# Kernel tuning notes

Hardware: AMD Instinct MI355X
Metric: run time of the kernel (lower is better)

## Reference

```python
import jax, jax.numpy as jnp
import numpy as np
from jax import lax

B, CIN, COUT, H, W = 4, 192, 192, 256, 256
K, S, P = 3, 1, 1


def setup_inputs() -> dict:
    key = jax.random.key(0)
    k1, k2, k3, k4 = jax.random.split(key, 4)
    x = jax.random.normal(k1, (B, CIN, H, W), dtype=jnp.float32)
    mask = jax.random.randint(k2, (B, 1, H, W), 0, 2, dtype=jnp.int32)
    fan_in = CIN * K * K
    bound = 1.0 / np.sqrt(fan_in)
    weight = jax.random.uniform(k3, (COUT, CIN, K, K), dtype=jnp.float32, minval=-bound, maxval=bound)
    bias = jax.random.uniform(k4, (COUT,), dtype=jnp.float32, minval=-bound, maxval=bound)
    return {"x": x, "mask": mask, "weight": weight, "bias": bias}


def reference(x, mask, weight, bias):
    # Dense conv (NCHW, OIHW). Equivalent to the unfold + matmul on gathered
    # patches; the custom scatter kernel writes results only at output
    # positions whose receptive field overlaps a nonzero mask entry,
    # leaving other positions zero.
    out = lax.conv_general_dilated(
        x, weight,
        window_strides=(S, S),
        padding=[(P, P), (P, P)],
        dimension_numbers=("NCHW", "OIHW", "NCHW"),
    ) + bias[None, :, None, None]

    # valid[b, 0, oh, ow] = any(mask patch != 0)  -> max-pool of (mask != 0)
    m = jnp.any(mask != 0, axis=1, keepdims=True).astype(out.dtype)  # [B,1,H,W]
    pooled = lax.reduce_window(
        m, 0.0, lax.max,
        window_dimensions=(1, 1, K, K),
        window_strides=(1, 1, S, S),
        padding=[(0, 0), (0, 0), (P, P), (P, P)],
    )  # [B,1,Hout,Wout]
    valid = (pooled > 0).astype(out.dtype)
    return out * valid
```

## Files before the change

### kernel.cpp

```cpp
#include <hip/hip_runtime.h>

typedef short short8 __attribute__((ext_vector_type(8)));
typedef __bf16 bf16x8 __attribute__((ext_vector_type(8)));
typedef float f32x4 __attribute__((ext_vector_type(4)));

#define HP 258

__device__ __forceinline__ short f2bf(float f) {
  unsigned u = __builtin_bit_cast(unsigned, f);
  unsigned r = u + 0x7fffu + ((u >> 16) & 1u);
  return (short)(r >> 16);
}

__device__ __forceinline__ void async16(void* l, const void* g) {
  __builtin_amdgcn_global_load_lds((const __attribute__((address_space(1))) void*)g,
                                   (__attribute__((address_space(3))) void*)l,
                                   16, 0, 0);
}

__global__ __launch_bounds__(256) void zero_border(short* __restrict__ Xp) {
  int gid = blockIdx.x * 256 + threadIdx.x;
  if (gid >= 4 * 1028 * 24) return;
  int g = gid % 24;
  int pix = gid / 24;
  int b = pix / 1028;
  int i = pix - b * 1028;
  int h, w;
  if (i < 258)      { h = 0;   w = i; }
  else if (i < 516) { h = 257; w = i - 258; }
  else { int j = i - 516; h = 1 + (j >> 1); w = (j & 1) ? 257 : 0; }
  short8 z = {0, 0, 0, 0, 0, 0, 0, 0};
  *(short8*)&Xp[(((size_t)b * HP + h) * HP + w) * 192 + g * 8] = z;
}

__global__ __launch_bounds__(256) void transpose_x(const float* __restrict__ x,
                                                   short* __restrict__ Xp) {
  __shared__ short lds[64 * 200];
  const int t = threadIdx.x;
  const int w = t & 63;
  const int g = t >> 6;
  const int w0 = blockIdx.x << 6;
  const int ih = blockIdx.y;
  const int b = blockIdx.z;
  const float* xb = x + ((size_t)b * 192) * 65536 + (size_t)ih * 256 + w0;
#pragma unroll
  for (int pass = 0; pass < 6; ++pass) {
    int ci = pass * 32 + g * 8;
    short8 v;
#pragma unroll
    for (int j = 0; j < 8; ++j) v[j] = f2bf(xb[(size_t)(ci + j) * 65536 + w]);
    *(short8*)&lds[w * 200 + ci] = v;
  }
  __syncthreads();
  short* dst = Xp + (((size_t)b * HP + (ih + 1)) * HP + (w0 + 1)) * 192;
#pragma unroll
  for (int i = 0; i < 6; ++i) {
    int gid = i * 256 + t;
    int ww = gid / 24;
    int c = gid - ww * 24;
    short8 vv = *(const short8*)&lds[ww * 200 + c * 8];
    *(short8*)&dst[(size_t)ww * 192 + c * 8] = vv;
  }
}

__global__ __launch_bounds__(256) void repack_w(const float* __restrict__ Wsrc,
                                                short* __restrict__ Wr) {
  int gid = blockIdx.x * 256 + threadIdx.x;
  if (gid >= 9 * 6 * 768) return;
  int gr = gid % 768;
  int tk = gid / 768;
  int kc = tk % 6;
  int tap = tk / 6;
  int co = gr >> 2;
  int q = (gr & 3) ^ (co & 3);
  int ci = kc * 32 + q * 8;
  short8 v;
#pragma unroll
  for (int j = 0; j < 8; ++j) v[j] = f2bf(Wsrc[(size_t)(co * 192 + ci + j) * 9 + tap]);
  *(short8*)&Wr[(size_t)gid * 8] = v;
}

__global__ __launch_bounds__(256) void valid_mask(const int* __restrict__ mask,
                                                  float* __restrict__ Vg) {
  int gid = blockIdx.x * 256 + threadIdx.x;
  int b = gid >> 16;
  int r = gid & 65535;
  int oh = r >> 8;
  int ow = r & 255;
  const int* mb = mask + ((size_t)b << 16);
  int any = 0;
  for (int dh = -1; dh <= 1; ++dh) {
    int h = oh + dh;
    if ((unsigned)h >= 256u) continue;
    for (int dw = -1; dw <= 1; ++dw) {
      int w = ow + dw;
      if ((unsigned)w >= 256u) continue;
      any |= (mb[h * 256 + w] != 0);
    }
  }
  Vg[gid] = any ? 1.0f : 0.0f;
}

__global__ __launch_bounds__(256) void conv_mfma(
    const short* __restrict__ Xp,
    const short* __restrict__ Wr,
    const float* __restrict__ Vg,
    const float* __restrict__ bias,
    float* __restrict__ out)
{
  __shared__ short Al[768 * 8];
  __shared__ short Bl[512 * 8];

  const int t = threadIdx.x;
  const int lane = t & 63;
  const int wave = t >> 6;
  const int quad = lane >> 4;
  const int l16 = lane & 15;

  const int b = blockIdx.z;
  const int oh = blockIdx.y;
  const int ow0 = blockIdx.x << 7;

  const int axor = quad ^ (l16 & 3);
  int aoff[3];
#pragma unroll
  for (int c = 0; c < 3; ++c) aoff[c] = ((wave * 48 + c * 16 + l16) * 4 + axor) * 8;
  int boff[8];
#pragma unroll
  for (int s = 0; s < 8; ++s) boff[s] = ((s * 16 + l16) * 4 + axor) * 8;

  const int p0 = t >> 2;
  const int q0 = (t & 3) ^ (p0 & 3);

  const f32x4 fzero = {0.f, 0.f, 0.f, 0.f};
  f32x4 acc[3][8];
#pragma unroll
  for (int c = 0; c < 3; ++c)
#pragma unroll
    for (int s = 0; s < 8; ++s) acc[c][s] = fzero;

  const short* Xb = Xp + (size_t)b * HP * HP * 192;

  for (int kh = 0; kh < 3; ++kh) {
    for (int kw = 0; kw < 3; ++kw) {
      const int tap = kh * 3 + kw;
      const short* Wt = Wr + (size_t)tap * 6 * 768 * 8;
      const short* Xrow = Xb + ((size_t)(oh + kh) * HP + (ow0 + kw)) * 192;
      const short* xs0 = Xrow + p0 * 192 + q0 * 8;
      for (int kc = 0; kc < 6; ++kc) {
        const short* wsrc = Wt + kc * (768 * 8) + t * 8;
        async16(&Al[t * 8], wsrc);
        async16(&Al[(t + 256) * 8], wsrc + 256 * 8);
        async16(&Al[(t + 512) * 8], wsrc + 512 * 8);
        const short* xsrc = xs0 + kc * 32;
        async16(&Bl[t * 8], xsrc);
        async16(&Bl[(t + 256) * 8], xsrc + 64 * 192);
        __syncthreads();

        short8 a[3], bb[8];
#pragma unroll
        for (int c = 0; c < 3; ++c) a[c] = *(const short8*)&Al[aoff[c]];
#pragma unroll
        for (int s = 0; s < 8; ++s) bb[s] = *(const short8*)&Bl[boff[s]];
#pragma unroll
        for (int c = 0; c < 3; ++c)
#pragma unroll
          for (int s = 0; s < 8; ++s)
            acc[c][s] = __builtin_amdgcn_mfma_f32_16x16x32_bf16(
                __builtin_bit_cast(bf16x8, a[c]), __builtin_bit_cast(bf16x8, bb[s]),
                acc[c][s], 0, 0, 0);
        __syncthreads();
      }
    }
  }

  float bv[3][4];
#pragma unroll
  for (int c = 0; c < 3; ++c)
#pragma unroll
    for (int r = 0; r < 4; ++r) bv[c][r] = bias[wave * 48 + c * 16 + quad * 4 + r];

  const float* vrow = Vg + ((size_t)b * 256 + oh) * 256 + ow0;
  float* ob = out + (size_t)(b * 192) * 65536 + (size_t)oh * 256 + ow0;
#pragma unroll
  for (int s = 0; s < 8; ++s) {
    float v = vrow[s * 16 + l16];
#pragma unroll
    for (int c = 0; c < 3; ++c) {
      int cobase = wave * 48 + c * 16 + quad * 4;
#pragma unroll
      for (int r = 0; r < 4; ++r)
        ob[(size_t)(cobase + r) * 65536 + s * 16 + l16] = (acc[c][s][r] + bv[c][r]) * v;
    }
  }
}

__global__ __launch_bounds__(256) void naive_conv(
    const float* __restrict__ x, const int* __restrict__ mask,
    const float* __restrict__ w, const float* __restrict__ bias,
    float* __restrict__ out) {
  size_t gid = (size_t)blockIdx.x * 256 + threadIdx.x;
  int ow = (int)(gid & 255);
  int oh = (int)((gid >> 8) & 255);
  int rest = (int)(gid >> 16);
  int co = rest % 192;
  int b = rest / 192;
  int any = 0;
  for (int dh = -1; dh <= 1; ++dh) {
    int h = oh + dh;
    if ((unsigned)h >= 256u) continue;
    for (int dw = -1; dw <= 1; ++dw) {
      int ww2 = ow + dw;
      if ((unsigned)ww2 >= 256u) continue;
      any |= (mask[((size_t)b << 16) + h * 256 + ww2] != 0);
    }
  }
  if (!any) { out[gid] = 0.f; return; }
  float acc = bias[co];
  const float* xb = x + (size_t)b * 192 * 65536;
  const float* wc = w + (size_t)co * 192 * 9;
  for (int ci = 0; ci < 192; ++ci) {
    const float* xc = xb + (size_t)ci * 65536;
    const float* wk = wc + ci * 9;
    for (int kh = 0; kh < 3; ++kh) {
      int h = oh + kh - 1;
      if ((unsigned)h >= 256u) continue;
      for (int kw = 0; kw < 3; ++kw) {
        int w2 = ow + kw - 1;
        if ((unsigned)w2 >= 256u) continue;
        acc += xc[h * 256 + w2] * wk[kh * 3 + kw];
      }
    }
  }
  out[gid] = acc;
}

extern "C" void kernel_launch(void* const* d_in, const int* in_sizes, int n_in,
                              void* d_out, int out_size, void* d_ws, size_t ws_size,
                              hipStream_t stream) {
  const float* x = (const float*)d_in[0];
  const int* mask = (const int*)d_in[1];
  const float* w = (const float*)d_in[2];
  const float* bias = (const float*)d_in[3];
  float* out = (float*)d_out;

  const size_t xp_bytes = (size_t)4 * HP * HP * 192 * 2;
  const size_t wr_bytes = (size_t)9 * 6 * 768 * 8 * 2;
  const size_t vg_bytes = (size_t)4 * 256 * 256 * 4;

  if (d_ws && ws_size >= xp_bytes + wr_bytes + vg_bytes) {
    short* Xp = (short*)d_ws;
    short* Wr = (short*)((char*)d_ws + xp_bytes);
    float* Vg = (float*)((char*)d_ws + xp_bytes + wr_bytes);
    zero_border<<<386, 256, 0, stream>>>(Xp);
    transpose_x<<<dim3(4, 256, 4), 256, 0, stream>>>(x, Xp);
    repack_w<<<162, 256, 0, stream>>>(w, Wr);
    valid_mask<<<1024, 256, 0, stream>>>(mask, Vg);
    conv_mfma<<<dim3(2, 256, 4), 256, 0, stream>>>(Xp, Wr, Vg, bias, out);
  } else {
    naive_conv<<<196608, 256, 0, stream>>>(x, mask, w, bias, out);
  }
}
```

Before: 556.0 us.

## Fuse prep kernels into one launch and double-buffer conv LDS staging

New measurement: 593.7 us. +6.8%, slower.

```diff
diff --git a/kernel.cpp b/kernel.cpp
--- a/kernel.cpp
+++ b/kernel.cpp
@@ -18,87 +18,97 @@
                                    16, 0, 0);
 }
 
-__global__ __launch_bounds__(256) void zero_border(short* __restrict__ Xp) {
-  int gid = blockIdx.x * 256 + threadIdx.x;
-  if (gid >= 4 * 1028 * 24) return;
-  int g = gid % 24;
-  int pix = gid / 24;
-  int b = pix / 1028;
-  int i = pix - b * 1028;
-  int h, w;
-  if (i < 258)      { h = 0;   w = i; }
-  else if (i < 516) { h = 257; w = i - 258; }
-  else { int j = i - 516; h = 1 + (j >> 1); w = (j & 1) ? 257 : 0; }
-  short8 z = {0, 0, 0, 0, 0, 0, 0, 0};
-  *(short8*)&Xp[(((size_t)b * HP + h) * HP + w) * 192 + g * 8] = z;
-}
-
-__global__ __launch_bounds__(256) void transpose_x(const float* __restrict__ x,
-                                                   short* __restrict__ Xp) {
+__global__ __launch_bounds__(256) void prepass(const float* __restrict__ x,
+                                               const int* __restrict__ mask,
+                                               const float* __restrict__ Wsrc,
+                                               short* __restrict__ Xp,
+                                               short* __restrict__ Wr,
+                                               float* __restrict__ Vg) {
   __shared__ short lds[64 * 200];
   const int t = threadIdx.x;
-  const int w = t & 63;
-  const int g = t >> 6;
-  const int w0 = blockIdx.x << 6;
-  const int ih = blockIdx.y;
-  const int b = blockIdx.z;
-  const float* xb = x + ((size_t)b * 192) * 65536 + (size_t)ih * 256 + w0;
-#pragma unroll
-  for (int pass = 0; pass < 6; ++pass) {
-    int ci = pass * 32 + g * 8;
+  const int bid = blockIdx.x;
+
+  if (bid < 4096) {
+    const int w = t & 63;
+    const int g = t >> 6;
+    const int w0 = (bid & 3) << 6;
+    const int ih = (bid >> 2) & 255;
+    const int b = bid >> 10;
+    const float* xb = x + ((size_t)b * 192) * 65536 + (size_t)ih * 256 + w0;
+#pragma unroll
+    for (int pass = 0; pass < 6; ++pass) {
+      int ci = pass * 32 + g * 8;
+      short8 v;
+#pragma unroll
+      for (int j = 0; j < 8; ++j) v[j] = f2bf(xb[(size_t)(ci + j) * 65536 + w]);
+      *(short8*)&lds[w * 200 + ci] = v;
+    }
+    __syncthreads();
+    short* dst = Xp + (((size_t)b * HP + (ih + 1)) * HP + (w0 + 1)) * 192;
+#pragma unroll
+    for (int i = 0; i < 6; ++i) {
+      int gid = i * 256 + t;
+      int ww = gid / 24;
+      int c = gid - ww * 24;
+      short8 vv = *(const short8*)&lds[ww * 200 + c * 8];
+      *(short8*)&dst[(size_t)ww * 192 + c * 8] = vv;
+    }
+    return;
+  }
+
+  int rb = bid - 4096;
+  if (rb < 386) {
+    int gid = rb * 256 + t;
+    if (gid >= 4 * 1028 * 24) return;
+    int g = gid % 24;
+    int pix = gid / 24;
+    int b = pix / 1028;
+    int i = pix - b * 1028;
+    int h, w;
+    if (i < 258)      { h = 0;   w = i; }
+    else if (i < 516) { h = 257; w = i - 258; }
+    else { int j = i - 516; h = 1 + (j >> 1); w = (j & 1) ? 257 : 0; }
+    short8 z = {0, 0, 0, 0, 0, 0, 0, 0};
+    *(short8*)&Xp[(((size_t)b * HP + h) * HP + w) * 192 + g * 8] = z;
+    return;
+  }
+  rb -= 386;
+  if (rb < 162) {
+    int gid = rb * 256 + t;
+    if (gid >= 9 * 6 * 768) return;
+    int gr = gid % 768;
+    int tk = gid / 768;
+    int kc = tk % 6;
+    int tap = tk / 6;
+    int co = gr >> 2;
+    int q = (gr & 3) ^ (co & 3);
+    int ci = kc * 32 + q * 8;
     short8 v;
 #pragma unroll
-    for (int j = 0; j < 8; ++j) v[j] = f2bf(xb[(size_t)(ci + j) * 65536 + w]);
-    *(short8*)&lds[w * 200 + ci] = v;
-  }
-  __syncthreads();
-  short* dst = Xp + (((size_t)b * HP + (ih + 1)) * HP + (w0 + 1)) * 192;
-#pragma unroll
-  for (int i = 0; i < 6; ++i) {
-    int gid = i * 256 + t;
-    int ww = gid / 24;
-    int c = gid - ww * 24;
-    short8 vv = *(const short8*)&lds[ww * 200 + c * 8];
-    *(short8*)&dst[(size_t)ww * 192 + c * 8] = vv;
-  }
-}
-
-__global__ __launch_bounds__(256) void repack_w(const float* __restrict__ Wsrc,
-                                                short* __restrict__ Wr) {
-  int gid = blockIdx.x * 256 + threadIdx.x;
-  if (gid >= 9 * 6 * 768) return;
-  int gr = gid % 768;
-  int tk = gid / 768;
-  int kc = tk % 6;
-  int tap = tk / 6;
-  int co = gr >> 2;
-  int q = (gr & 3) ^ (co & 3);
-  int ci = kc * 32 + q * 8;
-  short8 v;
-#pragma unroll
-  for (int j = 0; j < 8; ++j) v[j] = f2bf(Wsrc[(size_t)(co * 192 + ci + j) * 9 + tap]);
-  *(short8*)&Wr[(size_t)gid * 8] = v;
-}
-
-__global__ __launch_bounds__(256) void valid_mask(const int* __restrict__ mask,
-                                                  float* __restrict__ Vg) {
-  int gid = blockIdx.x * 256 + threadIdx.x;
-  int b = gid >> 16;
-  int r = gid & 65535;
-  int oh = r >> 8;
-  int ow = r & 255;
-  const int* mb = mask + ((size_t)b << 16);
-  int any = 0;
-  for (int dh = -1; dh <= 1; ++dh) {
-    int h = oh + dh;
-    if ((unsigned)h >= 256u) continue;
-    for (int dw = -1; dw <= 1; ++dw) {
-      int w = ow + dw;
-      if ((unsigned)w >= 256u) continue;
-      any |= (mb[h * 256 + w] != 0);
-    }
-  }
-  Vg[gid] = any ? 1.0f : 0.0f;
+    for (int j = 0; j < 8; ++j) v[j] = f2bf(Wsrc[(size_t)(co * 192 + ci + j) * 9 + tap]);
+    *(short8*)&Wr[(size_t)gid * 8] = v;
+    return;
+  }
+  rb -= 162;
+  {
+    int gid = rb * 256 + t;
+    int b = gid >> 16;
+    int r = gid & 65535;
+    int oh = r >> 8;
+    int ow = r & 255;
+    const int* mb = mask + ((size_t)b << 16);
+    int any = 0;
+    for (int dh = -1; dh <= 1; ++dh) {
+      int h = oh + dh;
+      if ((unsigned)h >= 256u) continue;
+      for (int dw = -1; dw <= 1; ++dw) {
+        int w = ow + dw;
+        if ((unsigned)w >= 256u) continue;
+        any |= (mb[h * 256 + w] != 0);
+      }
+    }
+    Vg[gid] = any ? 1.0f : 0.0f;
+  }
 }
 
 __global__ __launch_bounds__(256) void conv_mfma(
@@ -108,8 +118,8 @@
     const float* __restrict__ bias,
     float* __restrict__ out)
 {
-  __shared__ short Al[768 * 8];
-  __shared__ short Bl[512 * 8];
+  __shared__ short Al[2][768 * 8];
+  __shared__ short Bl[2][512 * 8];
 
   const int t = threadIdx.x;
   const int lane = t & 63;
@@ -118,7 +128,8 @@
   const int l16 = lane & 15;
 
   const int b = blockIdx.z;
-  const int oh = blockIdx.y;
+  const int by = blockIdx.y;
+  const int oh = ((by & 3) << 6) | (by >> 2);
   const int ow0 = blockIdx.x << 7;
 
   const int axor = quad ^ (l16 & 3);
@@ -131,6 +142,7 @@
 
   const int p0 = t >> 2;
   const int q0 = (t & 3) ^ (p0 & 3);
+  const int poff = p0 * 192 + q0 * 8;
 
   const f32x4 fzero = {0.f, 0.f, 0.f, 0.f};
   f32x4 acc[3][8];
@@ -141,37 +153,45 @@
 
   const short* Xb = Xp + (size_t)b * HP * HP * 192;
 
-  for (int kh = 0; kh < 3; ++kh) {
-    for (int kw = 0; kw < 3; ++kw) {
-      const int tap = kh * 3 + kw;
-      const short* Wt = Wr + (size_t)tap * 6 * 768 * 8;
-      const short* Xrow = Xb + ((size_t)(oh + kh) * HP + (ow0 + kw)) * 192;
-      const short* xs0 = Xrow + p0 * 192 + q0 * 8;
-      for (int kc = 0; kc < 6; ++kc) {
-        const short* wsrc = Wt + kc * (768 * 8) + t * 8;
-        async16(&Al[t * 8], wsrc);
-        async16(&Al[(t + 256) * 8], wsrc + 256 * 8);
-        async16(&Al[(t + 512) * 8], wsrc + 512 * 8);
-        const short* xsrc = xs0 + kc * 32;
-        async16(&Bl[t * 8], xsrc);
-        async16(&Bl[(t + 256) * 8], xsrc + 64 * 192);
-        __syncthreads();
-
-        short8 a[3], bb[8];
-#pragma unroll
-        for (int c = 0; c < 3; ++c) a[c] = *(const short8*)&Al[aoff[c]];
-#pragma unroll
-        for (int s = 0; s < 8; ++s) bb[s] = *(const short8*)&Bl[boff[s]];
-#pragma unroll
-        for (int c = 0; c < 3; ++c)
-#pragma unroll
-          for (int s = 0; s < 8; ++s)
-            acc[c][s] = __builtin_amdgcn_mfma_f32_16x16x32_bf16(
-                __builtin_bit_cast(bf16x8, a[c]), __builtin_bit_cast(bf16x8, bb[s]),
-                acc[c][s], 0, 0, 0);
-        __syncthreads();
-      }
-    }
+  auto stage = [&](int bs, int kh, int kw, int kc) {
+    const short* wsrc = Wr + ((size_t)(kh * 3 + kw) * 6 + kc) * (768 * 8) + t * 8;
+    async16(&Al[bs][t * 8], wsrc);
+    async16(&Al[bs][(t + 256) * 8], wsrc + 256 * 8);
+    async16(&Al[bs][(t + 512) * 8], wsrc + 512 * 8);
+    const short* xsrc = Xb + ((size_t)(oh + kh) * HP + (ow0 + kw)) * 192 + poff + kc * 32;
+    async16(&Bl[bs][t * 8], xsrc);
+    async16(&Bl[bs][(t + 256) * 8], xsrc + 64 * 192);
+  };
+
+  stage(0, 0, 0, 0);
+  __syncthreads();
+
+  int cur = 0;
+  for (int s = 0; s < 54; ++s) {
+    const int sn = s + 1;
+    if (sn < 54) {
+      const int tap = sn / 6;
+      const int kc = sn - tap * 6;
+      const int kh = tap / 3;
+      const int kw = tap - kh * 3;
+      stage(cur ^ 1, kh, kw, kc);
+    }
+    short8 a[3], bb[8];
+#pragma unroll
+    for (int c = 0; c < 3; ++c) a[c] = *(const short8*)&Al[cur][aoff[c]];
+#pragma unroll
+    for (int k = 0; k < 8; ++k) bb[k] = *(const short8*)&Bl[cur][boff[k]];
+    __builtin_amdgcn_s_setprio(1);
+#pragma unroll
+    for (int c = 0; c < 3; ++c)
+#pragma unroll
+      for (int k = 0; k < 8; ++k)
+        acc[c][k] = __builtin_amdgcn_mfma_f32_16x16x32_bf16(
+            __builtin_bit_cast(bf16x8, a[c]), __builtin_bit_cast(bf16x8, bb[k]),
+            acc[c][k], 0, 0, 0);
+    __builtin_amdgcn_s_setprio(0);
+    __syncthreads();
+    cur ^= 1;
   }
 
   float bv[3][4];
@@ -252,10 +272,7 @@
     short* Xp = (short*)d_ws;
     short* Wr = (short*)((char*)d_ws + xp_bytes);
     float* Vg = (float*)((char*)d_ws + xp_bytes + wr_bytes);
-    zero_border<<<386, 256, 0, stream>>>(Xp);
-    transpose_x<<<dim3(4, 256, 4), 256, 0, stream>>>(x, Xp);
-    repack_w<<<162, 256, 0, stream>>>(w, Wr);
-    valid_mask<<<1024, 256, 0, stream>>>(mask, Vg);
+    prepass<<<5668, 256, 0, stream>>>(x, mask, w, Xp, Wr, Vg);
     conv_mfma<<<dim3(2, 256, 4), 256, 0, stream>>>(Xp, Wr, Vg, bias, out);
   } else {
     naive_conv<<<196608, 256, 0, stream>>>(x, mask, w, bias, out);
```
